# Kernel tuning notes

Hardware: AMD Instinct MI355X
Metric: run time of the kernel (lower is better)

## Reference

```python
import jax, jax.numpy as jnp
import numpy as np
import math

N_NEURONS = 2048
MAX_MEMORY = 32
BATCH = 128

def setup_inputs() -> dict:
    key = jax.random.key(0)
    k1, k2, k3 = jax.random.split(key, 3)
    state_trace = jax.random.normal(k1, (BATCH, N_NEURONS, MAX_MEMORY), dtype=jnp.float32)
    fc1_weight = jax.random.normal(k2, (N_NEURONS, MAX_MEMORY, 256), dtype=jnp.float32) * math.sqrt(2.0 / MAX_MEMORY)
    fc1_bias = jnp.zeros((N_NEURONS, 256), dtype=jnp.float32)
    fc2_weight = jax.random.normal(k3, (N_NEURONS, 128, 2), dtype=jnp.float32) * math.sqrt(2.0 / 128)
    fc2_bias = jnp.zeros((N_NEURONS, 2), dtype=jnp.float32)
    T = jnp.ones((1,), dtype=jnp.float32)
    return {"state_trace": state_trace, "fc1_weight": fc1_weight, "fc1_bias": fc1_bias,
            "fc2_weight": fc2_weight, "fc2_bias": fc2_bias, "T": T}

def _glu(x):
    # torch F.glu(dim=-1): first half * sigmoid(second half)
    a, b = jnp.split(x, 2, axis=-1)
    return a * jax.nn.sigmoid(b)

def reference(state_trace, fc1_weight, fc1_bias, fc2_weight, fc2_bias, T):
    # per-neuron batched GEMM 1: (b,n,m) x (n,m,256) -> (b,n,256)
    x_fc1 = jnp.einsum('bnm,nmh->bnh', state_trace, fc1_weight) + fc1_bias
    x_glu1 = _glu(x_fc1)                                   # (b, n, 128)
    # per-neuron batched GEMM 2: (b,n,128) x (n,128,2) -> (b,n,2)
    x_fc2 = jnp.einsum('bnh,nho->bno', x_glu1, fc2_weight) + fc2_bias
    x_glu2 = _glu(x_fc2)                                   # (b, n, 1)
    return jnp.squeeze(x_glu2, -1) / T                     # (b, n)
```

## Files before the change

### kernel.cpp

```cpp
#include <hip/hip_runtime.h>
#include <hip/hip_bf16.h>


#define NN 2048

typedef __attribute__((ext_vector_type(8))) short short8;
typedef __attribute__((ext_vector_type(4))) float floatx4;
typedef __attribute__((ext_vector_type(4))) int int4v;

static __device__ __forceinline__ unsigned int pkbf(float a, float b) {
    __hip_bfloat162 h = __float22bfloat162_rn(make_float2(a, b));
    return *(unsigned int*)&h;
}

static __device__ __forceinline__ float sigmoidf_(float x) {
    return __builtin_amdgcn_rcpf(1.0f + __expf(-x));
}

static __device__ __forceinline__ void gload_lds16(const float* g, float* l) {
    __builtin_amdgcn_global_load_lds((const __attribute__((address_space(1))) void*)g,
                                     (__attribute__((address_space(3))) void*)l,
                                     16, 0, 0);
}

__global__ __launch_bounds__(512, 4)
void nlm_kernel(const float* __restrict__ st,
                const float* __restrict__ w1,
                const float* __restrict__ b1,
                const float* __restrict__ w2,
                const float* __restrict__ b2,
                const float* __restrict__ Tp,
                float* __restrict__ out_t)
{
    const int n = blockIdx.x;
    const int t = threadIdx.x;

    __shared__ __align__(16) float  ldsW[32 * 256];
    __shared__ float4 ldsP[128];
    __shared__ float  ldsO[128];
    short* ldsB = (short*)ldsW;

    const int lane = t & 63;
    const int wv   = t >> 6;
    const int m    = lane & 15;
    const int quad = lane >> 4;

    {
        const float* gW = w1 + (size_t)n * 8192;
        #pragma unroll
        for (int i = 0; i < 4; ++i) {
            const int off = wv * 1024 + i * 256;
            gload_lds16(gW + off + lane * 4, &ldsW[off]);
        }
    }

    floatx4 av[2];
    {
        const int b = wv * 16 + m;
        const float* sp = st + (size_t)b * (NN * 32) + (size_t)n * 32 + quad * 8;
        av[0] = *(const floatx4*)sp;
        av[1] = *(const floatx4*)(sp + 4);
    }

    if (t < 128) {
        const float* b1p = b1 + n * 256;
        const float* w2p = w2 + n * 256;
        float  pba = b1p[t];
        float  pbb = b1p[128 + t];
        float2 pw2 = *(const float2*)(w2p + 2 * t);
        ldsP[t] = make_float4(pba, pbb, pw2.x, pw2.y);
    }

    const float bb0  = b2[n * 2 + 0];
    const float bb1  = b2[n * 2 + 1];
    const float invT = 1.0f / Tp[0];

    short8 afrag;
    {
        union { int4v i; short8 s; } u;
        u.i[0] = pkbf(av[0][0], av[0][1]);
        u.i[1] = pkbf(av[0][2], av[0][3]);
        u.i[2] = pkbf(av[1][0], av[1][1]);
        u.i[3] = pkbf(av[1][2], av[1][3]);
        afrag = u.s;
    }

    __syncthreads();

    float w[16];
    const int h  = t & 255;
    const int kb = (t >> 8) * 16;
    #pragma unroll
    for (int k = 0; k < 16; ++k)
        w[k] = ldsW[(kb + k) * 256 + h];

    __syncthreads();

    {
        const int base = ((h >> 4) * 512) + ((h & 15) * 8) + (t >> 8) * 256;
        #pragma unroll
        for (int q = 0; q < 2; ++q) {
            union { int4v i; short8 s; } u;
            #pragma unroll
            for (int e = 0; e < 4; ++e)
                u.i[e] = pkbf(w[q * 8 + 2 * e], w[q * 8 + 2 * e + 1]);
            *(short8*)&ldsB[base + q * 128] = u.s;
        }
    }

    __syncthreads();

    float pacc[4][2];
    #pragma unroll
    for (int r = 0; r < 4; ++r)
        pacc[r][0] = pacc[r][1] = 0.0f;

    #pragma unroll
    for (int p = 0; p < 8; ++p) {
        short8 bfA = *(short8*)&ldsB[(p * 64 + lane) * 8];
        short8 bfB = *(short8*)&ldsB[((p + 8) * 64 + lane) * 8];
        float4 prm = ldsP[p * 16 + m];
        floatx4 ca = {prm.x, prm.x, prm.x, prm.x};
        floatx4 cb = {prm.y, prm.y, prm.y, prm.y};

        floatx4 xa = __builtin_amdgcn_mfma_f32_16x16x32_bf16(afrag, bfA, ca, 0, 0, 0);
        floatx4 xb = __builtin_amdgcn_mfma_f32_16x16x32_bf16(afrag, bfB, cb, 0, 0, 0);
        #pragma unroll
        for (int r = 0; r < 4; ++r) {
            float glu = xa[r] * sigmoidf_(xb[r]);
            pacc[r][0] += glu * prm.z;
            pacc[r][1] += glu * prm.w;
        }
    }

    #pragma unroll
    for (int r = 0; r < 4; ++r) {
        float s0 = pacc[r][0];
        float s1 = pacc[r][1];
        s0 += __shfl_xor(s0, 1);  s1 += __shfl_xor(s1, 1);
        s0 += __shfl_xor(s0, 2);  s1 += __shfl_xor(s1, 2);
        s0 += __shfl_xor(s0, 4);  s1 += __shfl_xor(s1, 4);
        s0 += __shfl_xor(s0, 8);  s1 += __shfl_xor(s1, 8);
        if (m == 0) {
            const int b = wv * 16 + quad * 4 + r;
            float x0 = s0 + bb0;
            float x1 = s1 + bb1;
            ldsO[b] = x0 * sigmoidf_(x1) * invT;
        }
    }

    __syncthreads();

    if (t < 128)
        out_t[(size_t)n * 128 + t] = ldsO[t];
}

__global__ __launch_bounds__(256)
void transpose_kernel(const float* __restrict__ out_t, float* __restrict__ out)
{
    __shared__ float tile[32][33];
    const int t    = threadIdx.x;
    const int bidx = blockIdx.x;
    const int n0   = (bidx & 63) * 32;
    const int b0   = (bidx >> 6) * 32;

    const int tx = t & 31;
    const int ty = t >> 5;

    #pragma unroll
    for (int i = 0; i < 4; ++i) {
        const int nl = ty + i * 8;
        tile[nl][tx] = out_t[(size_t)(n0 + nl) * 128 + b0 + tx];
    }

    __syncthreads();

    #pragma unroll
    for (int i = 0; i < 4; ++i) {
        const int bl = ty + i * 8;
        out[(size_t)(b0 + bl) * NN + n0 + tx] = tile[tx][bl];
    }
}

extern "C" void kernel_launch(void* const* d_in, const int* in_sizes, int n_in,
                              void* d_out, int out_size, void* d_ws, size_t ws_size,
                              hipStream_t stream) {
    const float* st = (const float*)d_in[0];
    const float* w1 = (const float*)d_in[1];
    const float* b1 = (const float*)d_in[2];
    const float* w2 = (const float*)d_in[3];
    const float* b2 = (const float*)d_in[4];
    const float* T  = (const float*)d_in[5];
    float* out   = (float*)d_out;
    float* out_t = (float*)d_ws;

    nlm_kernel<<<dim3(NN), dim3(512), 0, stream>>>(st, w1, b1, w2, b2, T, out_t);
    transpose_kernel<<<dim3(256), dim3(256), 0, stream>>>(out_t, out);
}
```

Baseline: 131.5 us.

## Process four neurons per block with double-buffered weight prefetch

Each block now handles four consecutive neurons instead of one. While the current neuron is being computed, it prefetches the next neuron's fc1 weights into a second LDS buffer with async global-to-LDS loads, and loads the next state fragment, biases and fc2 weights into registers. The aim is to hide global-load latency behind the MFMA and GLU work and to cut per-block launch and setup cost. In exchange, LDS per block doubles, which limits how many blocks fit on a CU, and the grid shrinks to a quarter of its size.

Measured after the change: 161.0 us. +22.5%, slower.

```diff
diff --git a/kernel.cpp b/kernel.cpp
--- a/kernel.cpp
+++ b/kernel.cpp
@@ -3,6 +3,8 @@
 
 
 #define NN 2048
+#define NPB 4
+#define GRID (NN / NPB)
 
 typedef __attribute__((ext_vector_type(8))) short short8;
 typedef __attribute__((ext_vector_type(4))) float floatx4;
@@ -21,6 +23,15 @@
     __builtin_amdgcn_global_load_lds((const __attribute__((address_space(1))) void*)g,
                                      (__attribute__((address_space(3))) void*)l,
                                      16, 0, 0);
+}
+
+static __device__ __forceinline__ short8 pack_afrag(floatx4 a0, floatx4 a1) {
+    union { int4v i; short8 s; } u;
+    u.i[0] = pkbf(a0[0], a0[1]);
+    u.i[1] = pkbf(a0[2], a0[3]);
+    u.i[2] = pkbf(a1[0], a1[1]);
+    u.i[3] = pkbf(a1[2], a1[3]);
+    return u.s;
 }
 
 __global__ __launch_bounds__(512, 4)
@@ -32,127 +43,156 @@
                 const float* __restrict__ Tp,
                 float* __restrict__ out_t)
 {
-    const int n = blockIdx.x;
-    const int t = threadIdx.x;
-
-    __shared__ __align__(16) float  ldsW[32 * 256];
-    __shared__ float4 ldsP[128];
+    const int t  = threadIdx.x;
+    const int n0 = blockIdx.x * NPB;
+
+    __shared__ __align__(16) float  ldsW[2][32 * 256];
+    __shared__ float4 ldsP[2][128];
     __shared__ float  ldsO[128];
-    short* ldsB = (short*)ldsW;
 
     const int lane = t & 63;
     const int wv   = t >> 6;
     const int m    = lane & 15;
     const int quad = lane >> 4;
 
-    {
-        const float* gW = w1 + (size_t)n * 8192;
-        #pragma unroll
-        for (int i = 0; i < 4; ++i) {
-            const int off = wv * 1024 + i * 256;
-            gload_lds16(gW + off + lane * 4, &ldsW[off]);
-        }
-    }
-
-    floatx4 av[2];
+    const int h      = t & 255;
+    const int kh     = t >> 8;
+    const int cvbase = ((h >> 4) * 512) + ((h & 15) * 8) + kh * 256;
+
+    float pba = 0.f, pbb = 0.f; float2 pw2 = make_float2(0.f, 0.f);
+    if (t < 128) {
+        pba = b1[(size_t)n0 * 256 + t];
+        pbb = b1[(size_t)n0 * 256 + 128 + t];
+        pw2 = *(const float2*)(w2 + (size_t)n0 * 256 + 2 * t);
+    }
+    floatx4 av0, av1;
     {
         const int b = wv * 16 + m;
-        const float* sp = st + (size_t)b * (NN * 32) + (size_t)n * 32 + quad * 8;
-        av[0] = *(const floatx4*)sp;
-        av[1] = *(const floatx4*)(sp + 4);
-    }
-
-    if (t < 128) {
-        const float* b1p = b1 + n * 256;
-        const float* w2p = w2 + n * 256;
-        float  pba = b1p[t];
-        float  pbb = b1p[128 + t];
-        float2 pw2 = *(const float2*)(w2p + 2 * t);
-        ldsP[t] = make_float4(pba, pbb, pw2.x, pw2.y);
-    }
-
-    const float bb0  = b2[n * 2 + 0];
-    const float bb1  = b2[n * 2 + 1];
+        const float* sp = st + (size_t)b * (NN * 32) + (size_t)n0 * 32 + quad * 8;
+        av0 = *(const floatx4*)sp;
+        av1 = *(const floatx4*)(sp + 4);
+    }
+    {
+        const float* gW = w1 + (size_t)n0 * 8192;
+        #pragma unroll
+        for (int i2 = 0; i2 < 4; ++i2) {
+            const int off = wv * 1024 + i2 * 256;
+            gload_lds16(gW + off + lane * 4, &ldsW[0][off]);
+        }
+    }
+    float bb0 = b2[n0 * 2 + 0];
+    float bb1 = b2[n0 * 2 + 1];
     const float invT = 1.0f / Tp[0];
-
-    short8 afrag;
-    {
-        union { int4v i; short8 s; } u;
-        u.i[0] = pkbf(av[0][0], av[0][1]);
-        u.i[1] = pkbf(av[0][2], av[0][3]);
-        u.i[2] = pkbf(av[1][0], av[1][1]);
-        u.i[3] = pkbf(av[1][2], av[1][3]);
-        afrag = u.s;
-    }
+    if (t < 128) ldsP[0][t] = make_float4(pba, pbb, pw2.x, pw2.y);
+    short8 afrag = pack_afrag(av0, av1);
 
     __syncthreads();
 
-    float w[16];
-    const int h  = t & 255;
-    const int kb = (t >> 8) * 16;
     #pragma unroll
-    for (int k = 0; k < 16; ++k)
-        w[k] = ldsW[(kb + k) * 256 + h];
-
-    __syncthreads();
-
-    {
-        const int base = ((h >> 4) * 512) + ((h & 15) * 8) + (t >> 8) * 256;
+    for (int i = 0; i < NPB; ++i) {
+        const int cur = i & 1, nxt = cur ^ 1;
+        const int n = n0 + i;
+        const bool hn = (i + 1 < NPB);
+        short* ldsBc = (short*)ldsW[cur];
+
+        float npa = 0.f, npb_ = 0.f; float2 npw = make_float2(0.f, 0.f);
+        floatx4 nav0 = {0,0,0,0}, nav1 = {0,0,0,0};
+        float nbb0 = 0.f, nbb1 = 0.f;
+        if (hn) {
+            if (t < 128) {
+                npa  = b1[(size_t)(n + 1) * 256 + t];
+                npb_ = b1[(size_t)(n + 1) * 256 + 128 + t];
+                npw  = *(const float2*)(w2 + (size_t)(n + 1) * 256 + 2 * t);
+            }
+            const int b = wv * 16 + m;
+            const float* sp = st + (size_t)b * (NN * 32) + (size_t)(n + 1) * 32 + quad * 8;
+            nav0 = *(const floatx4*)sp;
+            nav1 = *(const floatx4*)(sp + 4);
+            nbb0 = b2[(n + 1) * 2 + 0];
+            nbb1 = b2[(n + 1) * 2 + 1];
+            const float* gW = w1 + (size_t)(n + 1) * 8192;
+            #pragma unroll
+            for (int i2 = 0; i2 < 4; ++i2) {
+                const int off = wv * 1024 + i2 * 256;
+                gload_lds16(gW + off + lane * 4, &ldsW[nxt][off]);
+            }
+        }
+
+        float w[16];
+        #pragma unroll
+        for (int k = 0; k < 16; ++k)
+            w[k] = ldsW[cur][(kh * 16 + k) * 256 + h];
+
+        asm volatile("s_waitcnt lgkmcnt(0)" ::: "memory");
+        __builtin_amdgcn_s_barrier();
+        __builtin_amdgcn_sched_barrier(0);
+
         #pragma unroll
         for (int q = 0; q < 2; ++q) {
-            union { int4v i; short8 s; } u;
+            union { int4v iv; short8 s; } u;
             #pragma unroll
             for (int e = 0; e < 4; ++e)
-                u.i[e] = pkbf(w[q * 8 + 2 * e], w[q * 8 + 2 * e + 1]);
-            *(short8*)&ldsB[base + q * 128] = u.s;
-        }
-    }
-
-    __syncthreads();
-
-    float pacc[4][2];
-    #pragma unroll
-    for (int r = 0; r < 4; ++r)
-        pacc[r][0] = pacc[r][1] = 0.0f;
-
-    #pragma unroll
-    for (int p = 0; p < 8; ++p) {
-        short8 bfA = *(short8*)&ldsB[(p * 64 + lane) * 8];
-        short8 bfB = *(short8*)&ldsB[((p + 8) * 64 + lane) * 8];
-        float4 prm = ldsP[p * 16 + m];
-        floatx4 ca = {prm.x, prm.x, prm.x, prm.x};
-        floatx4 cb = {prm.y, prm.y, prm.y, prm.y};
-
-        floatx4 xa = __builtin_amdgcn_mfma_f32_16x16x32_bf16(afrag, bfA, ca, 0, 0, 0);
-        floatx4 xb = __builtin_amdgcn_mfma_f32_16x16x32_bf16(afrag, bfB, cb, 0, 0, 0);
+                u.iv[e] = pkbf(w[q * 8 + 2 * e], w[q * 8 + 2 * e + 1]);
+            *(short8*)&ldsBc[cvbase + q * 128] = u.s;
+        }
+        short8 nafrag = afrag;
+        if (hn) nafrag = pack_afrag(nav0, nav1);
+
+        asm volatile("s_waitcnt lgkmcnt(0)" ::: "memory");
+        __builtin_amdgcn_s_barrier();
+        __builtin_amdgcn_sched_barrier(0);
+
+        float pacc[4][2];
+        #pragma unroll
+        for (int r = 0; r < 4; ++r)
+            pacc[r][0] = pacc[r][1] = 0.0f;
+
+        #pragma unroll
+        for (int p = 0; p < 8; ++p) {
+            short8 bfA = *(short8*)&ldsBc[(p * 64 + lane) * 8];
+            short8 bfB = *(short8*)&ldsBc[((p + 8) * 64 + lane) * 8];
+            float4 prm = ldsP[cur][p * 16 + m];
+            floatx4 ca = {prm.x, prm.x, prm.x, prm.x};
+            floatx4 cb = {prm.y, prm.y, prm.y, prm.y};
+            floatx4 xa = __builtin_amdgcn_mfma_f32_16x16x32_bf16(afrag, bfA, ca, 0, 0, 0);
+            floatx4 xb = __builtin_amdgcn_mfma_f32_16x16x32_bf16(afrag, bfB, cb, 0, 0, 0);
+            #pragma unroll
+            for (int r = 0; r < 4; ++r) {
+                float glu = xa[r] * sigmoidf_(xb[r]);
+                pacc[r][0] += glu * prm.z;
+                pacc[r][1] += glu * prm.w;
+            }
+        }
+
         #pragma unroll
         for (int r = 0; r < 4; ++r) {
-            float glu = xa[r] * sigmoidf_(xb[r]);
-            pacc[r][0] += glu * prm.z;
-            pacc[r][1] += glu * prm.w;
-        }
-    }
-
-    #pragma unroll
-    for (int r = 0; r < 4; ++r) {
-        float s0 = pacc[r][0];
-        float s1 = pacc[r][1];
-        s0 += __shfl_xor(s0, 1);  s1 += __shfl_xor(s1, 1);
-        s0 += __shfl_xor(s0, 2);  s1 += __shfl_xor(s1, 2);
-        s0 += __shfl_xor(s0, 4);  s1 += __shfl_xor(s1, 4);
-        s0 += __shfl_xor(s0, 8);  s1 += __shfl_xor(s1, 8);
-        if (m == 0) {
-            const int b = wv * 16 + quad * 4 + r;
-            float x0 = s0 + bb0;
-            float x1 = s1 + bb1;
-            ldsO[b] = x0 * sigmoidf_(x1) * invT;
-        }
-    }
-
-    __syncthreads();
-
-    if (t < 128)
-        out_t[(size_t)n * 128 + t] = ldsO[t];
+            float s0 = pacc[r][0];
+            float s1 = pacc[r][1];
+            s0 += __shfl_xor(s0, 1);  s1 += __shfl_xor(s1, 1);
+            s0 += __shfl_xor(s0, 2);  s1 += __shfl_xor(s1, 2);
+            s0 += __shfl_xor(s0, 4);  s1 += __shfl_xor(s1, 4);
+            s0 += __shfl_xor(s0, 8);  s1 += __shfl_xor(s1, 8);
+            if (m == 0) {
+                const int b = wv * 16 + quad * 4 + r;
+                float x0 = s0 + bb0;
+                float x1 = s1 + bb1;
+                ldsO[b] = x0 * sigmoidf_(x1) * invT;
+            }
+        }
+        if (hn && t < 128)
+            ldsP[nxt][t] = make_float4(npa, npb_, npw.x, npw.y);
+
+        asm volatile("s_waitcnt vmcnt(0) lgkmcnt(0)" ::: "memory");
+        __builtin_amdgcn_s_barrier();
+        __builtin_amdgcn_sched_barrier(0);
+
+        if (t < 128)
+            out_t[(size_t)n * 128 + t] = ldsO[t];
+
+        afrag = nafrag;
+        bb0 = nbb0;
+        bb1 = nbb1;
+    }
 }
 
 __global__ __launch_bounds__(256)
@@ -194,6 +234,6 @@
     float* out   = (float*)d_out;
     float* out_t = (float*)d_ws;
 
-    nlm_kernel<<<dim3(NN), dim3(512), 0, stream>>>(st, w1, b1, w2, b2, T, out_t);
+    nlm_kernel<<<dim3(GRID), dim3(512), 0, stream>>>(st, w1, b1, w2, b2, T, out_t);
     transpose_kernel<<<dim3(256), dim3(256), 0, stream>>>(out_t, out);
 }
```

## Use one wavefront per neuron with register-resident bf16 weight fragments

Applied to the files above, without the earlier changes.

The block shrinks from 8 waves to a single 64-thread wave per neuron. Each lane now loads its fc1 weight fragments straight from global memory into registers and packs them to bf16, which removes the LDS staging, the transpose and two barriers. The wave then loops over the 8 batch tiles and reuses those fragments for every tile. In exchange there are strided scalar global loads for the weights, more registers per thread, and less parallelism per block, with more serial work per wave.

New measurement: 211.0 us. +60.5%, slower.

```diff
diff --git a/kernel.cpp b/kernel.cpp
--- a/kernel.cpp
+++ b/kernel.cpp
@@ -17,13 +17,16 @@
     return __builtin_amdgcn_rcpf(1.0f + __expf(-x));
 }
 
-static __device__ __forceinline__ void gload_lds16(const float* g, float* l) {
-    __builtin_amdgcn_global_load_lds((const __attribute__((address_space(1))) void*)g,
-                                     (__attribute__((address_space(3))) void*)l,
-                                     16, 0, 0);
+static __device__ __forceinline__ short8 pack_afrag(floatx4 a0, floatx4 a1) {
+    union { int4v i; short8 s; } u;
+    u.i[0] = pkbf(a0[0], a0[1]);
+    u.i[1] = pkbf(a0[2], a0[3]);
+    u.i[2] = pkbf(a1[0], a1[1]);
+    u.i[3] = pkbf(a1[2], a1[3]);
+    return u.s;
 }
 
-__global__ __launch_bounds__(512, 4)
+__global__ __launch_bounds__(64, 4)
 void nlm_kernel(const float* __restrict__ st,
                 const float* __restrict__ w1,
                 const float* __restrict__ b1,
@@ -32,127 +35,97 @@
                 const float* __restrict__ Tp,
                 float* __restrict__ out_t)
 {
-    const int n = blockIdx.x;
-    const int t = threadIdx.x;
-
-    __shared__ __align__(16) float  ldsW[32 * 256];
-    __shared__ float4 ldsP[128];
-    __shared__ float  ldsO[128];
-    short* ldsB = (short*)ldsW;
-
-    const int lane = t & 63;
-    const int wv   = t >> 6;
+    const int n    = blockIdx.x;
+    const int lane = threadIdx.x;
     const int m    = lane & 15;
     const int quad = lane >> 4;
 
+    __shared__ float4 ldsP[128];
+    __shared__ float  ldsO[128];
+
     {
-        const float* gW = w1 + (size_t)n * 8192;
+        const float* b1p = b1 + (size_t)n * 256;
+        const float* w2p = w2 + (size_t)n * 256;
         #pragma unroll
-        for (int i = 0; i < 4; ++i) {
-            const int off = wv * 1024 + i * 256;
-            gload_lds16(gW + off + lane * 4, &ldsW[off]);
+        for (int j = 0; j < 2; ++j) {
+            const int hh = lane + 64 * j;
+            ldsP[hh] = make_float4(b1p[hh], b1p[128 + hh],
+                                   w2p[2 * hh], w2p[2 * hh + 1]);
         }
     }
-
-    floatx4 av[2];
-    {
-        const int b = wv * 16 + m;
-        const float* sp = st + (size_t)b * (NN * 32) + (size_t)n * 32 + quad * 8;
-        av[0] = *(const floatx4*)sp;
-        av[1] = *(const floatx4*)(sp + 4);
-    }
-
-    if (t < 128) {
-        const float* b1p = b1 + n * 256;
-        const float* w2p = w2 + n * 256;
-        float  pba = b1p[t];
-        float  pbb = b1p[128 + t];
-        float2 pw2 = *(const float2*)(w2p + 2 * t);
-        ldsP[t] = make_float4(pba, pbb, pw2.x, pw2.y);
-    }
-
     const float bb0  = b2[n * 2 + 0];
     const float bb1  = b2[n * 2 + 1];
     const float invT = 1.0f / Tp[0];
 
-    short8 afrag;
+    short8 wf[16];
     {
-        union { int4v i; short8 s; } u;
-        u.i[0] = pkbf(av[0][0], av[0][1]);
-        u.i[1] = pkbf(av[0][2], av[0][3]);
-        u.i[2] = pkbf(av[1][0], av[1][1]);
-        u.i[3] = pkbf(av[1][2], av[1][3]);
-        afrag = u.s;
-    }
-
-    __syncthreads();
-
-    float w[16];
-    const int h  = t & 255;
-    const int kb = (t >> 8) * 16;
-    #pragma unroll
-    for (int k = 0; k < 16; ++k)
-        w[k] = ldsW[(kb + k) * 256 + h];
-
-    __syncthreads();
-
-    {
-        const int base = ((h >> 4) * 512) + ((h & 15) * 8) + (t >> 8) * 256;
+        const float* gW = w1 + (size_t)n * 8192 + (size_t)(quad * 8) * 256 + m;
         #pragma unroll
-        for (int q = 0; q < 2; ++q) {
+        for (int p = 0; p < 16; ++p) {
+            float v[8];
+            #pragma unroll
+            for (int e = 0; e < 8; ++e)
+                v[e] = gW[e * 256 + p * 16];
             union { int4v i; short8 s; } u;
-            #pragma unroll
-            for (int e = 0; e < 4; ++e)
-                u.i[e] = pkbf(w[q * 8 + 2 * e], w[q * 8 + 2 * e + 1]);
-            *(short8*)&ldsB[base + q * 128] = u.s;
+            u.i[0] = pkbf(v[0], v[1]);
+            u.i[1] = pkbf(v[2], v[3]);
+            u.i[2] = pkbf(v[4], v[5]);
+            u.i[3] = pkbf(v[6], v[7]);
+            wf[p] = u.s;
         }
     }
 
     __syncthreads();
 
-    float pacc[4][2];
-    #pragma unroll
-    for (int r = 0; r < 4; ++r)
-        pacc[r][0] = pacc[r][1] = 0.0f;
+    #pragma unroll 2
+    for (int mt = 0; mt < 8; ++mt) {
+        const int b = mt * 16 + m;
+        const float* sp = st + (size_t)b * (NN * 32) + (size_t)n * 32 + quad * 8;
+        floatx4 a0 = *(const floatx4*)sp;
+        floatx4 a1 = *(const floatx4*)(sp + 4);
+        short8 afrag = pack_afrag(a0, a1);
 
-    #pragma unroll
-    for (int p = 0; p < 8; ++p) {
-        short8 bfA = *(short8*)&ldsB[(p * 64 + lane) * 8];
-        short8 bfB = *(short8*)&ldsB[((p + 8) * 64 + lane) * 8];
-        float4 prm = ldsP[p * 16 + m];
-        floatx4 ca = {prm.x, prm.x, prm.x, prm.x};
-        floatx4 cb = {prm.y, prm.y, prm.y, prm.y};
+        float pacc[4][2];
+        #pragma unroll
+        for (int r = 0; r < 4; ++r)
+            pacc[r][0] = pacc[r][1] = 0.0f;
 
-        floatx4 xa = __builtin_amdgcn_mfma_f32_16x16x32_bf16(afrag, bfA, ca, 0, 0, 0);
-        floatx4 xb = __builtin_amdgcn_mfma_f32_16x16x32_bf16(afrag, bfB, cb, 0, 0, 0);
+        #pragma unroll
+        for (int p = 0; p < 8; ++p) {
+            float4 prm = ldsP[p * 16 + m];
+            floatx4 ca = {prm.x, prm.x, prm.x, prm.x};
+            floatx4 cb = {prm.y, prm.y, prm.y, prm.y};
+            floatx4 xa = __builtin_amdgcn_mfma_f32_16x16x32_bf16(afrag, wf[p],     ca, 0, 0, 0);
+            floatx4 xb = __builtin_amdgcn_mfma_f32_16x16x32_bf16(afrag, wf[p + 8], cb, 0, 0, 0);
+            #pragma unroll
+            for (int r = 0; r < 4; ++r) {
+                float glu = xa[r] * sigmoidf_(xb[r]);
+                pacc[r][0] += glu * prm.z;
+                pacc[r][1] += glu * prm.w;
+            }
+        }
+
         #pragma unroll
         for (int r = 0; r < 4; ++r) {
-            float glu = xa[r] * sigmoidf_(xb[r]);
-            pacc[r][0] += glu * prm.z;
-            pacc[r][1] += glu * prm.w;
-        }
-    }
-
-    #pragma unroll
-    for (int r = 0; r < 4; ++r) {
-        float s0 = pacc[r][0];
-        float s1 = pacc[r][1];
-        s0 += __shfl_xor(s0, 1);  s1 += __shfl_xor(s1, 1);
-        s0 += __shfl_xor(s0, 2);  s1 += __shfl_xor(s1, 2);
-        s0 += __shfl_xor(s0, 4);  s1 += __shfl_xor(s1, 4);
-        s0 += __shfl_xor(s0, 8);  s1 += __shfl_xor(s1, 8);
-        if (m == 0) {
-            const int b = wv * 16 + quad * 4 + r;
-            float x0 = s0 + bb0;
-            float x1 = s1 + bb1;
-            ldsO[b] = x0 * sigmoidf_(x1) * invT;
+            float s0 = pacc[r][0];
+            float s1 = pacc[r][1];
+            s0 += __shfl_xor(s0, 1);  s1 += __shfl_xor(s1, 1);
+            s0 += __shfl_xor(s0, 2);  s1 += __shfl_xor(s1, 2);
+            s0 += __shfl_xor(s0, 4);  s1 += __shfl_xor(s1, 4);
+            s0 += __shfl_xor(s0, 8);  s1 += __shfl_xor(s1, 8);
+            if (m == 0) {
+                const int b_out = mt * 16 + quad * 4 + r;
+                float x0 = s0 + bb0;
+                float x1 = s1 + bb1;
+                ldsO[b_out] = x0 * sigmoidf_(x1) * invT;
+            }
         }
     }
 
     __syncthreads();
 
-    if (t < 128)
-        out_t[(size_t)n * 128 + t] = ldsO[t];
+    out_t[(size_t)n * 128 + lane]      = ldsO[lane];
+    out_t[(size_t)n * 128 + 64 + lane] = ldsO[64 + lane];
 }
 
 __global__ __launch_bounds__(256)
@@ -194,6 +167,6 @@
     float* out   = (float*)d_out;
     float* out_t = (float*)d_ws;
 
-    nlm_kernel<<<dim3(NN), dim3(512), 0, stream>>>(st, w1, b1, w2, b2, T, out_t);
+    nlm_kernel<<<dim3(NN), dim3(64), 0, stream>>>(st, w1, b1, w2, b2, T, out_t);
     transpose_kernel<<<dim3(256), dim3(256), 0, stream>>>(out_t, out);
 }
```

## Pre-transpose state trace to bf16 per-neuron layout in a separate kernel

Applied to the files above, without the earlier changes.

Adds a pre-pass kernel that converts state_trace to bf16 and rearranges it so each neuron's MFMA A-fragments sit contiguously. The main kernel then does one coalesced 16-byte load per lane instead of strided fp32 gathers across the batch. It also lowers the occupancy hint in launch_bounds from 4 to 2. The cost is an extra kernel launch and an extra write and read of a 16 MB bf16 buffer in workspace.

Measured after the change: 154.9 us. 1.18x slower.

```diff
diff --git a/kernel.cpp b/kernel.cpp
--- a/kernel.cpp
+++ b/kernel.cpp
@@ -23,8 +23,34 @@
                                      16, 0, 0);
 }
 
-__global__ __launch_bounds__(512, 4)
-void nlm_kernel(const float* __restrict__ st,
+__global__ __launch_bounds__(256)
+void st_transpose_kernel(const float* __restrict__ st, short* __restrict__ st_t)
+{
+    const int g = blockIdx.x;
+    const int t = threadIdx.x;
+    const int b  = g & 127;
+    const int n  = (g >> 7) * 256 + t;
+    const int mt = b >> 4;
+    const int m  = b & 15;
+
+    const float* src = st + (size_t)b * (NN * 32) + (size_t)n * 32;
+    short* dst = st_t + (size_t)n * 4096 + mt * 512 + m * 8;
+
+    #pragma unroll
+    for (int q = 0; q < 4; ++q) {
+        floatx4 a0 = *(const floatx4*)(src + q * 8);
+        floatx4 a1 = *(const floatx4*)(src + q * 8 + 4);
+        union { int4v i; short8 s; } u;
+        u.i[0] = pkbf(a0[0], a0[1]);
+        u.i[1] = pkbf(a0[2], a0[3]);
+        u.i[2] = pkbf(a1[0], a1[1]);
+        u.i[3] = pkbf(a1[2], a1[3]);
+        *(short8*)(dst + q * 128) = u.s;
+    }
+}
+
+__global__ __launch_bounds__(512, 2)
+void nlm_kernel(const short* __restrict__ st_t,
                 const float* __restrict__ w1,
                 const float* __restrict__ b1,
                 const float* __restrict__ w2,
@@ -54,17 +80,11 @@
         }
     }
 
-    floatx4 av[2];
-    {
-        const int b = wv * 16 + m;
-        const float* sp = st + (size_t)b * (NN * 32) + (size_t)n * 32 + quad * 8;
-        av[0] = *(const floatx4*)sp;
-        av[1] = *(const floatx4*)(sp + 4);
-    }
+    short8 afrag = *(const short8*)(st_t + (size_t)n * 4096 + wv * 512 + lane * 8);
 
     if (t < 128) {
-        const float* b1p = b1 + n * 256;
-        const float* w2p = w2 + n * 256;
+        const float* b1p = b1 + (size_t)n * 256;
+        const float* w2p = w2 + (size_t)n * 256;
         float  pba = b1p[t];
         float  pbb = b1p[128 + t];
         float2 pw2 = *(const float2*)(w2p + 2 * t);
@@ -75,35 +95,25 @@
     const float bb1  = b2[n * 2 + 1];
     const float invT = 1.0f / Tp[0];
 
-    short8 afrag;
-    {
-        union { int4v i; short8 s; } u;
-        u.i[0] = pkbf(av[0][0], av[0][1]);
-        u.i[1] = pkbf(av[0][2], av[0][3]);
-        u.i[2] = pkbf(av[1][0], av[1][1]);
-        u.i[3] = pkbf(av[1][2], av[1][3]);
-        afrag = u.s;
-    }
-
     __syncthreads();
 
     float w[16];
     const int h  = t & 255;
-    const int kb = (t >> 8) * 16;
+    const int kh = t >> 8;
     #pragma unroll
     for (int k = 0; k < 16; ++k)
-        w[k] = ldsW[(kb + k) * 256 + h];
+        w[k] = ldsW[(kh * 16 + k) * 256 + h];
 
     __syncthreads();
 
     {
-        const int base = ((h >> 4) * 512) + ((h & 15) * 8) + (t >> 8) * 256;
+        const int base = ((h >> 4) * 512) + ((h & 15) * 8) + kh * 256;
         #pragma unroll
         for (int q = 0; q < 2; ++q) {
-            union { int4v i; short8 s; } u;
+            union { int4v iv; short8 s; } u;
             #pragma unroll
             for (int e = 0; e < 4; ++e)
-                u.i[e] = pkbf(w[q * 8 + 2 * e], w[q * 8 + 2 * e + 1]);
+                u.iv[e] = pkbf(w[q * 8 + 2 * e], w[q * 8 + 2 * e + 1]);
             *(short8*)&ldsB[base + q * 128] = u.s;
         }
     }
@@ -122,7 +132,6 @@
         float4 prm = ldsP[p * 16 + m];
         floatx4 ca = {prm.x, prm.x, prm.x, prm.x};
         floatx4 cb = {prm.y, prm.y, prm.y, prm.y};
-
         floatx4 xa = __builtin_amdgcn_mfma_f32_16x16x32_bf16(afrag, bfA, ca, 0, 0, 0);
         floatx4 xb = __builtin_amdgcn_mfma_f32_16x16x32_bf16(afrag, bfB, cb, 0, 0, 0);
         #pragma unroll
@@ -193,7 +202,9 @@
     const float* T  = (const float*)d_in[5];
     float* out   = (float*)d_out;
     float* out_t = (float*)d_ws;
-
-    nlm_kernel<<<dim3(NN), dim3(512), 0, stream>>>(st, w1, b1, w2, b2, T, out_t);
+    short* st_t  = (short*)((char*)d_ws + (2u << 20));
+
+    st_transpose_kernel<<<dim3(1024), dim3(256), 0, stream>>>(st, st_t);
+    nlm_kernel<<<dim3(NN), dim3(512), 0, stream>>>(st_t, w1, b1, w2, b2, T, out_t);
     transpose_kernel<<<dim3(256), dim3(256), 0, stream>>>(out_t, out);
 }
```
